# Kernel tuning notes

Hardware: AMD Instinct MI355X
Metric: run time of the kernel (lower is better)

The kernel has to match this reference:

```python
import jax, jax.numpy as jnp
import numpy as np

B, T, C, H = 16, 2048, 1024, 128  # BATCH_SIZE, BLOCK_SIZE, EMBEDDING_SIZE, HEAD_SIZE


def setup_inputs() -> dict:
    key = jax.random.key(0)
    kx, kk, kq, kv = jax.random.split(key, 4)
    x = jax.random.normal(kx, (B, T, C), dtype=jnp.float32)
    # torch Linear(C, H, bias=False): y = x @ W^T with W [H, C]; we store W^T as [C, H]
    scale = C ** -0.5
    Wk = jax.random.normal(kk, (C, H), dtype=jnp.float32) * scale
    Wq = jax.random.normal(kq, (C, H), dtype=jnp.float32) * scale
    Wv = jax.random.normal(kv, (C, H), dtype=jnp.float32) * scale
    return {"x": x, "Wk": Wk, "Wq": Wq, "Wv": Wv}


def reference(x, Wk, Wq, Wv):
    # projections: [B, T, H]
    k = jnp.einsum("btc,ch->bth", x, Wk)
    q = jnp.einsum("btc,ch->bth", x, Wq)
    v = jnp.einsum("btc,ch->bth", x, Wv)
    # scaled scores: [B, T, T]
    scores = jnp.einsum("bqh,bkh->bqk", q, k) * (H ** -0.5)
    # causal mask (tril) then softmax over keys
    causal = jnp.tril(jnp.ones((T, T), dtype=bool))
    scores = jnp.where(causal, scores, -jnp.inf)
    weights = jax.nn.softmax(scores, axis=-1)
    # dropout with p=0.0 is identity (eval mode)
    return jnp.einsum("bqk,bkh->bqh", weights, v)
```

## Files before the change

kernel.cpp:

```cpp
#include <hip/hip_runtime.h>
#include <cmath>

#define B_ 16
#define T_ 2048
#define C_ 1024
#define H_ 128

#define BQ 64
#define BK 64
#define PS 68

#define PM 64
#define PK 64

typedef __bf16 bf16;
typedef bf16 bf16x8 __attribute__((ext_vector_type(8)));
typedef bf16 bf16x4 __attribute__((ext_vector_type(4)));
typedef float f32x4 __attribute__((ext_vector_type(4)));

#define GL_LDS16(gptr, lptr)                                                     \
    __builtin_amdgcn_global_load_lds(                                            \
        (const __attribute__((address_space(1))) unsigned int*)(gptr),           \
        (__attribute__((address_space(3))) unsigned int*)(lptr), 16, 0, 0)

__global__ __launch_bounds__(256) void convert_w(
    const float* __restrict__ Wq, const float* __restrict__ Wk,
    const float* __restrict__ Wv, bf16* __restrict__ wt)
{
    int gid = blockIdx.x * 256 + threadIdx.x;
    int w   = gid >> 14;
    int rem = gid & 16383;
    int n   = rem >> 7;
    int k0  = (rem & 127) * 8;
    const float* src = (w == 0) ? Wq : (w == 1) ? Wk : Wv;
    bf16x8 o;
#pragma unroll
    for (int j = 0; j < 8; ++j) o[j] = (bf16)src[(size_t)(k0 + j) * H_ + n];
    *(bf16x8*)(wt + (size_t)w * (H_ * C_) + (size_t)n * C_ + k0) = o;
}

__global__ __launch_bounds__(256, 2) void proj_mfma(
    const float* __restrict__ x, const bf16* __restrict__ wt,
    bf16* __restrict__ qb, bf16* __restrict__ kb, bf16* __restrict__ vtp)
{
    __shared__ bf16 xs[PM * PK];
    __shared__ bf16 ws[3 * H_ * PK];

    const int tid  = threadIdx.x;
    const int wave = tid >> 6;
    const int lane = tid & 63;
    const int quad = lane >> 4;
    const int lq   = lane & 15;
    const int wr   = wave >> 1;
    const int wc   = wave & 1;
    const int m0   = blockIdx.x * PM;

    f32x4 acc[3][2][4];
#pragma unroll
    for (int w = 0; w < 3; ++w)
#pragma unroll
        for (int mt = 0; mt < 2; ++mt)
#pragma unroll
            for (int nt = 0; nt < 4; ++nt)
                acc[w][mt][nt] = (f32x4){0.f, 0.f, 0.f, 0.f};

    int woff[12];
#pragma unroll
    for (int j = 0; j < 12; ++j) {
        int s  = (wave * 12 + j) * 64 + lane;
        int w  = s >> 10;
        int n  = (s >> 3) & 127;
        int cs = s & 7;
        int c  = cs ^ (n & 7);
        woff[j] = w * (H_ * C_) + n * C_ + c * 8;
    }
    int xoff[4], xslot[4];
#pragma unroll
    for (int j = 0; j < 4; ++j) {
        int f4  = j * 256 + tid;
        int row = f4 >> 4;
        int c4  = f4 & 15;
        int c   = c4 >> 1, half = c4 & 1;
        xoff[j]  = (m0 + row) * C_ + c4 * 4;
        xslot[j] = (row * 8 + (c ^ (row & 7))) * 8 + half * 4;
    }

    for (int k0 = 0; k0 < C_; k0 += PK) {
        __syncthreads();
#pragma unroll
        for (int j = 0; j < 12; ++j) {
            GL_LDS16(wt + woff[j] + k0, (char*)ws + (wave * 12 + j) * 1024);
        }
#pragma unroll
        for (int j = 0; j < 4; ++j) {
            float4 v = *(const float4*)(x + (size_t)xoff[j] + k0);
            bf16x4 o = {(bf16)v.x, (bf16)v.y, (bf16)v.z, (bf16)v.w};
            *(bf16x4*)&xs[xslot[j]] = o;
        }
        __syncthreads();

#pragma unroll
        for (int kc = 0; kc < 2; ++kc) {
            const int c = kc * 4 + quad;
            bf16x8 af[2];
#pragma unroll
            for (int mt = 0; mt < 2; ++mt) {
                int row  = wr * 32 + mt * 16 + lq;
                int slot = row * 8 + (c ^ (row & 7));
                af[mt] = *(const bf16x8*)&xs[slot * 8];
            }
#pragma unroll
            for (int w = 0; w < 3; ++w) {
#pragma unroll
                for (int nt = 0; nt < 4; ++nt) {
                    int n    = wc * 64 + nt * 16 + lq;
                    int slot = n * 8 + (c ^ (n & 7));
                    bf16x8 bfr = *(const bf16x8*)&ws[w * (H_ * PK) + slot * 8];
                    acc[w][0][nt] = __builtin_amdgcn_mfma_f32_16x16x32_bf16(af[0], bfr, acc[w][0][nt], 0, 0, 0);
                    acc[w][1][nt] = __builtin_amdgcn_mfma_f32_16x16x32_bf16(af[1], bfr, acc[w][1][nt], 0, 0, 0);
                }
            }
        }
    }

    const int b  = m0 >> 11;
    const int t0 = m0 & (T_ - 1);
#pragma unroll
    for (int w = 0; w < 2; ++w) {
        bf16* dst = (w == 0) ? qb : kb;
#pragma unroll
        for (int mt = 0; mt < 2; ++mt)
#pragma unroll
            for (int nt = 0; nt < 4; ++nt)
#pragma unroll
                for (int r = 0; r < 4; ++r) {
                    int row = m0 + wr * 32 + mt * 16 + quad * 4 + r;
                    int h   = wc * 64 + nt * 16 + lq;
                    dst[(size_t)row * H_ + h] = (bf16)acc[w][mt][nt][r];
                }
    }
#pragma unroll
    for (int mt = 0; mt < 2; ++mt)
#pragma unroll
        for (int nt = 0; nt < 4; ++nt) {
            int h = wc * 64 + nt * 16 + lq;
            int t = t0 + wr * 32 + mt * 16 + quad * 4;
            bf16x4 o = {(bf16)acc[2][mt][nt][0], (bf16)acc[2][mt][nt][1],
                        (bf16)acc[2][mt][nt][2], (bf16)acc[2][mt][nt][3]};
            *(bf16x4*)&vtp[((size_t)b * H_ + h) * T_ + t] = o;
        }
}

__global__ __launch_bounds__(256) void attn_mfma(
    const bf16* __restrict__ qb, const bf16* __restrict__ kb,
    const bf16* __restrict__ vt, float* __restrict__ out)
{
    __shared__ bf16 Ks[2][BK * 128];
    __shared__ bf16 Vs[2][128 * BK];
    __shared__ bf16 Ps[4][16 * PS];

    const int tid  = threadIdx.x;
    const int wave = tid >> 6;
    const int lane = tid & 63;
    const int quad = lane >> 4;
    const int lq   = lane & 15;

    const int bid = blockIdx.x;
    const int b   = bid & 15;
    const int jq  = bid >> 4;
    const int t0b = (31 - jq) * BQ;
    const int qt0 = t0b + wave * 16;

    const bf16* qrow = qb + ((size_t)b * T_ + qt0 + lq) * H_ + quad * 8;
    bf16x8 qf[4];
#pragma unroll
    for (int c = 0; c < 4; ++c) qf[c] = *(const bf16x8*)(qrow + 32 * c);

    f32x4 acc[8];
#pragma unroll
    for (int i = 0; i < 8; ++i) acc[i] = (f32x4){0.f, 0.f, 0.f, 0.f};
    f32x4 l_acc = (f32x4){0.f, 0.f, 0.f, 0.f};

    bf16x8 ones;
#pragma unroll
    for (int j = 0; j < 8; ++j) ones[j] = (bf16)1.0f;

    const float SC2 = 0.12751749985029928f;
    const int ntiles = t0b / BK + 1;

    const bf16* Kg = kb + (size_t)b * T_ * H_;
    const bf16* Vg = vt + (size_t)b * H_ * T_;
    bf16* Pw = &Ps[wave][0];

    int koff[4], voff[4], dst8[4];
#pragma unroll
    for (int j = 0; j < 4; ++j) {
        int p   = (j * 4 + wave) * 64 + lane;
        int r   = p >> 4, pos = p & 15;
        int l   = (pos & 8) | ((pos & 7) ^ (r & 7));
        koff[j] = r * H_ + l * 8;
        int hh  = p >> 3, pos2 = p & 7;
        voff[j] = hh * T_ + (pos2 ^ (hh & 7)) * 8;
        dst8[j] = (j * 4 + wave) * 64 * 8;
    }
    int swk[4], swv[2];
#pragma unroll
    for (int c = 0; c < 4; ++c) {
        int l = quad + 4 * c;
        swk[c] = (l & 8) | ((l & 7) ^ (lq & 7));
    }
#pragma unroll
    for (int kc = 0; kc < 2; ++kc) swv[kc] = (quad + 4 * kc) ^ (lq & 7);

#pragma unroll
    for (int j = 0; j < 4; ++j) {
        GL_LDS16(Kg + (size_t)koff[j], &Ks[0][dst8[j]]);
        GL_LDS16(Vg + (size_t)voff[j], &Vs[0][dst8[j]]);
    }

    for (int kt = 0; kt < ntiles; ++kt) {
        __syncthreads();
        if (kt + 1 < ntiles) {
            const int k1 = (kt + 1) * BK;
            const int nb = (kt + 1) & 1;
#pragma unroll
            for (int j = 0; j < 4; ++j) {
                GL_LDS16(Kg + (size_t)k1 * H_ + koff[j], &Ks[nb][dst8[j]]);
                GL_LDS16(Vg + (size_t)(k1 + voff[j]),    &Vs[nb][dst8[j]]);
            }
        }
        const bf16* Kb = &Ks[kt & 1][0];
        const bf16* Vb = &Vs[kt & 1][0];
        const bool finalt = (kt == ntiles - 1);

#pragma unroll
        for (int ns = 0; ns < 4; ++ns) {
            if (!finalt || ns <= wave) {
                f32x4 sv = (f32x4){0.f, 0.f, 0.f, 0.f};
#pragma unroll
                for (int c = 0; c < 4; ++c) {
                    bf16x8 kf = *(const bf16x8*)&Kb[((ns * 16 + lq) * 16 + swk[c]) * 8];
                    sv = __builtin_amdgcn_mfma_f32_16x16x32_bf16(qf[c], kf, sv, 0, 0, 0);
                }
                if (finalt && ns == wave) {
#pragma unroll
                    for (int r = 0; r < 4; ++r) {
                        float p = (lq <= quad * 4 + r) ? exp2f(sv[r] * SC2) : 0.f;
                        Pw[(quad * 4 + r) * PS + ns * 16 + lq] = (bf16)p;
                    }
                } else {
#pragma unroll
                    for (int r = 0; r < 4; ++r) {
                        Pw[(quad * 4 + r) * PS + ns * 16 + lq] = (bf16)exp2f(sv[r] * SC2);
                    }
                }
            } else {
#pragma unroll
                for (int r = 0; r < 4; ++r)
                    Pw[(quad * 4 + r) * PS + ns * 16 + lq] = (bf16)0.f;
            }
        }

        bf16x8 pf[2];
#pragma unroll
        for (int kc = 0; kc < 2; ++kc)
            pf[kc] = *(const bf16x8*)&Pw[lq * PS + kc * 32 + quad * 8];

        l_acc = __builtin_amdgcn_mfma_f32_16x16x32_bf16(pf[0], ones, l_acc, 0, 0, 0);
        l_acc = __builtin_amdgcn_mfma_f32_16x16x32_bf16(pf[1], ones, l_acc, 0, 0, 0);

#pragma unroll
        for (int ht = 0; ht < 8; ++ht) {
#pragma unroll
            for (int kc = 0; kc < 2; ++kc) {
                bf16x8 vf = *(const bf16x8*)&Vb[((ht * 16 + lq) * 8 + swv[kc]) * 8];
                acc[ht] = __builtin_amdgcn_mfma_f32_16x16x32_bf16(pf[kc], vf, acc[ht], 0, 0, 0);
            }
        }
    }

    float inv[4];
#pragma unroll
    for (int r = 0; r < 4; ++r) inv[r] = 1.f / l_acc[r];
#pragma unroll
    for (int ht = 0; ht < 8; ++ht) {
#pragma unroll
        for (int r = 0; r < 4; ++r) {
            out[((size_t)b * T_ + qt0 + quad * 4 + r) * H_ + ht * 16 + lq] = acc[ht][r] * inv[r];
        }
    }
}

extern "C" void kernel_launch(void* const* d_in, const int* in_sizes, int n_in,
                              void* d_out, int out_size, void* d_ws, size_t ws_size,
                              hipStream_t stream) {
    const float* x  = (const float*)d_in[0];
    const float* Wk = (const float*)d_in[1];
    const float* Wq = (const float*)d_in[2];
    const float* Wv = (const float*)d_in[3];
    float* out = (float*)d_out;

    bf16* qb = (bf16*)d_ws;
    bf16* kb = qb + (size_t)B_ * T_ * H_;
    bf16* vt = kb + (size_t)B_ * T_ * H_;
    bf16* wt = vt + (size_t)B_ * T_ * H_;

    convert_w<<<192, 256, 0, stream>>>(Wq, Wk, Wv, wt);

    proj_mfma<<<(B_ * T_) / PM, 256, 0, stream>>>(x, wt, qb, kb, vt);

    attn_mfma<<<(T_ / BQ) * B_, 256, 0, stream>>>(qb, kb, vt, out);
}
```

Baseline: 278.7 us.

## Double-buffer projection kernel LDS tiles with register and async prefetch

Converts the QKV projection kernel's K-loop to a two-stage pipeline. Weight tiles for the next step are loaded into the alternate LDS buffer with global_load_lds, and x tiles are prefetched into registers and stored after the MFMA work. This drops one barrier per iteration and overlaps memory traffic with compute. Doubling the shared memory lowers the launch bound from two blocks per CU to one, which reduces occupancy.

```diff
diff --git a/kernel.cpp b/kernel.cpp
--- a/kernel.cpp
+++ b/kernel.cpp
@@ -39,12 +39,12 @@
     *(bf16x8*)(wt + (size_t)w * (H_ * C_) + (size_t)n * C_ + k0) = o;
 }
 
-__global__ __launch_bounds__(256, 2) void proj_mfma(
+__global__ __launch_bounds__(256, 1) void proj_mfma(
     const float* __restrict__ x, const bf16* __restrict__ wt,
     bf16* __restrict__ qb, bf16* __restrict__ kb, bf16* __restrict__ vtp)
 {
-    __shared__ bf16 xs[PM * PK];
-    __shared__ bf16 ws[3 * H_ * PK];
+    __shared__ bf16 xs[2][PM * PK];
+    __shared__ bf16 ws[2][3 * H_ * PK];
 
     const int tid  = threadIdx.x;
     const int wave = tid >> 6;
@@ -85,19 +85,33 @@
         xslot[j] = (row * 8 + (c ^ (row & 7))) * 8 + half * 4;
     }
 
-    for (int k0 = 0; k0 < C_; k0 += PK) {
+    float4 xv[4];
+#pragma unroll
+    for (int j = 0; j < 4; ++j) xv[j] = *(const float4*)(x + (size_t)xoff[j]);
+#pragma unroll
+    for (int j = 0; j < 12; ++j)
+        GL_LDS16(wt + woff[j], (char*)ws[0] + (wave * 12 + j) * 1024);
+#pragma unroll
+    for (int j = 0; j < 4; ++j) {
+        bf16x4 o = {(bf16)xv[j].x, (bf16)xv[j].y, (bf16)xv[j].z, (bf16)xv[j].w};
+        *(bf16x4*)&xs[0][xslot[j]] = o;
+    }
+
+    const int NT = C_ / PK;
+    for (int kt = 0; kt < NT; ++kt) {
         __syncthreads();
-#pragma unroll
-        for (int j = 0; j < 12; ++j) {
-            GL_LDS16(wt + woff[j] + k0, (char*)ws + (wave * 12 + j) * 1024);
-        }
-#pragma unroll
-        for (int j = 0; j < 4; ++j) {
-            float4 v = *(const float4*)(x + (size_t)xoff[j] + k0);
-            bf16x4 o = {(bf16)v.x, (bf16)v.y, (bf16)v.z, (bf16)v.w};
-            *(bf16x4*)&xs[xslot[j]] = o;
-        }
-        __syncthreads();
+        const int cur = kt & 1;
+        const bool pf = (kt + 1 < NT);
+
+        if (pf) {
+            const int k1 = (kt + 1) * PK;
+#pragma unroll
+            for (int j = 0; j < 4; ++j)
+                xv[j] = *(const float4*)(x + (size_t)xoff[j] + k1);
+#pragma unroll
+            for (int j = 0; j < 12; ++j)
+                GL_LDS16(wt + woff[j] + k1, (char*)ws[cur ^ 1] + (wave * 12 + j) * 1024);
+        }
 
 #pragma unroll
         for (int kc = 0; kc < 2; ++kc) {
@@ -107,7 +121,7 @@
             for (int mt = 0; mt < 2; ++mt) {
                 int row  = wr * 32 + mt * 16 + lq;
                 int slot = row * 8 + (c ^ (row & 7));
-                af[mt] = *(const bf16x8*)&xs[slot * 8];
+                af[mt] = *(const bf16x8*)&xs[cur][slot * 8];
             }
 #pragma unroll
             for (int w = 0; w < 3; ++w) {
@@ -115,10 +129,18 @@
                 for (int nt = 0; nt < 4; ++nt) {
                     int n    = wc * 64 + nt * 16 + lq;
                     int slot = n * 8 + (c ^ (n & 7));
-                    bf16x8 bfr = *(const bf16x8*)&ws[w * (H_ * PK) + slot * 8];
+                    bf16x8 bfr = *(const bf16x8*)&ws[cur][w * (H_ * PK) + slot * 8];
                     acc[w][0][nt] = __builtin_amdgcn_mfma_f32_16x16x32_bf16(af[0], bfr, acc[w][0][nt], 0, 0, 0);
                     acc[w][1][nt] = __builtin_amdgcn_mfma_f32_16x16x32_bf16(af[1], bfr, acc[w][1][nt], 0, 0, 0);
                 }
+            }
+        }
+
+        if (pf) {
+#pragma unroll
+            for (int j = 0; j < 4; ++j) {
+                bf16x4 o = {(bf16)xv[j].x, (bf16)xv[j].y, (bf16)xv[j].z, (bf16)xv[j].w};
+                *(bf16x4*)&xs[cur ^ 1][xslot[j]] = o;
             }
         }
     }
```

After: 311.5 us. +11.7%, slower.

## Double-buffer weight tiles and load x directly into MFMA fragments in projection

Applied to the files above, without the earlier changes.

Restructures the projection GEMM loop to use a 32-wide K step with double-buffered LDS for the weights. The next tile is prefetched through async global-to-LDS loads and register prefetch of x, so one barrier per step replaces two. x no longer goes through LDS: each lane loads its fp32 A-fragment directly, converts it to bf16 in registers, and feeds the MFMA. This aims to overlap memory with compute, but it halves the work per barrier, doubles the iteration count, and raises register pressure.

```diff
diff --git a/kernel.cpp b/kernel.cpp
--- a/kernel.cpp
+++ b/kernel.cpp
@@ -11,7 +11,7 @@
 #define PS 68
 
 #define PM 64
-#define PK 64
+#define PKW 32
 
 typedef __bf16 bf16;
 typedef bf16 bf16x8 __attribute__((ext_vector_type(8)));
@@ -43,8 +43,7 @@
     const float* __restrict__ x, const bf16* __restrict__ wt,
     bf16* __restrict__ qb, bf16* __restrict__ kb, bf16* __restrict__ vtp)
 {
-    __shared__ bf16 xs[PM * PK];
-    __shared__ bf16 ws[3 * H_ * PK];
+    __shared__ bf16 ws[2][3 * H_ * PKW];
 
     const int tid  = threadIdx.x;
     const int wave = tid >> 6;
@@ -64,63 +63,75 @@
             for (int nt = 0; nt < 4; ++nt)
                 acc[w][mt][nt] = (f32x4){0.f, 0.f, 0.f, 0.f};
 
-    int woff[12];
-#pragma unroll
-    for (int j = 0; j < 12; ++j) {
-        int s  = (wave * 12 + j) * 64 + lane;
-        int w  = s >> 10;
-        int n  = (s >> 3) & 127;
-        int cs = s & 7;
-        int c  = cs ^ (n & 7);
+    int woff[6];
+#pragma unroll
+    for (int j = 0; j < 6; ++j) {
+        int p  = (wave * 6 + j) * 64 + lane;
+        int ng = p >> 2;
+        int cs = p & 3;
+        int w  = ng >> 7;
+        int n  = ng & 127;
+        int sn = (n ^ (n >> 2)) & 3;
+        int c  = cs ^ sn;
         woff[j] = w * (H_ * C_) + n * C_ + c * 8;
     }
-    int xoff[4], xslot[4];
-#pragma unroll
-    for (int j = 0; j < 4; ++j) {
-        int f4  = j * 256 + tid;
-        int row = f4 >> 4;
-        int c4  = f4 & 15;
-        int c   = c4 >> 1, half = c4 & 1;
-        xoff[j]  = (m0 + row) * C_ + c4 * 4;
-        xslot[j] = (row * 8 + (c ^ (row & 7))) * 8 + half * 4;
-    }
-
-    for (int k0 = 0; k0 < C_; k0 += PK) {
+    int xoff[2];
+#pragma unroll
+    for (int mt = 0; mt < 2; ++mt)
+        xoff[mt] = (m0 + wr * 32 + mt * 16 + lq) * C_ + quad * 8;
+
+    float4 xr[2][2], xr2[2][2];
+#pragma unroll
+    for (int mt = 0; mt < 2; ++mt)
+#pragma unroll
+        for (int h = 0; h < 2; ++h)
+            xr[mt][h] = *(const float4*)(x + (size_t)xoff[mt] + h * 4);
+#pragma unroll
+    for (int j = 0; j < 6; ++j)
+        GL_LDS16(wt + woff[j], (char*)ws[0] + (wave * 6 + j) * 1024);
+
+    const int NT = C_ / PKW;
+    for (int kt = 0; kt < NT; ++kt) {
         __syncthreads();
-#pragma unroll
-        for (int j = 0; j < 12; ++j) {
-            GL_LDS16(wt + woff[j] + k0, (char*)ws + (wave * 12 + j) * 1024);
-        }
-#pragma unroll
-        for (int j = 0; j < 4; ++j) {
-            float4 v = *(const float4*)(x + (size_t)xoff[j] + k0);
-            bf16x4 o = {(bf16)v.x, (bf16)v.y, (bf16)v.z, (bf16)v.w};
-            *(bf16x4*)&xs[xslot[j]] = o;
-        }
-        __syncthreads();
-
-#pragma unroll
-        for (int kc = 0; kc < 2; ++kc) {
-            const int c = kc * 4 + quad;
-            bf16x8 af[2];
-#pragma unroll
-            for (int mt = 0; mt < 2; ++mt) {
-                int row  = wr * 32 + mt * 16 + lq;
-                int slot = row * 8 + (c ^ (row & 7));
-                af[mt] = *(const bf16x8*)&xs[slot * 8];
+        const int cur = kt & 1;
+        if (kt + 1 < NT) {
+            const int k1 = (kt + 1) * PKW;
+#pragma unroll
+            for (int mt = 0; mt < 2; ++mt)
+#pragma unroll
+                for (int h = 0; h < 2; ++h)
+                    xr2[mt][h] = *(const float4*)(x + (size_t)xoff[mt] + k1 + h * 4);
+#pragma unroll
+            for (int j = 0; j < 6; ++j)
+                GL_LDS16(wt + woff[j] + k1, (char*)ws[cur ^ 1] + (wave * 6 + j) * 1024);
+        }
+
+        bf16x8 af[2];
+#pragma unroll
+        for (int mt = 0; mt < 2; ++mt) {
+            af[mt][0] = (bf16)xr[mt][0].x; af[mt][1] = (bf16)xr[mt][0].y;
+            af[mt][2] = (bf16)xr[mt][0].z; af[mt][3] = (bf16)xr[mt][0].w;
+            af[mt][4] = (bf16)xr[mt][1].x; af[mt][5] = (bf16)xr[mt][1].y;
+            af[mt][6] = (bf16)xr[mt][1].z; af[mt][7] = (bf16)xr[mt][1].w;
+        }
+
+#pragma unroll
+        for (int w = 0; w < 3; ++w)
+#pragma unroll
+            for (int nt = 0; nt < 4; ++nt) {
+                int n    = wc * 64 + nt * 16 + lq;
+                int sn   = (n ^ (n >> 2)) & 3;
+                int slot = (w * 128 + n) * 4 + (quad ^ sn);
+                bf16x8 bfr = *(const bf16x8*)&ws[cur][slot * 8];
+                acc[w][0][nt] = __builtin_amdgcn_mfma_f32_16x16x32_bf16(af[0], bfr, acc[w][0][nt], 0, 0, 0);
+                acc[w][1][nt] = __builtin_amdgcn_mfma_f32_16x16x32_bf16(af[1], bfr, acc[w][1][nt], 0, 0, 0);
             }
-#pragma unroll
-            for (int w = 0; w < 3; ++w) {
-#pragma unroll
-                for (int nt = 0; nt < 4; ++nt) {
-                    int n    = wc * 64 + nt * 16 + lq;
-                    int slot = n * 8 + (c ^ (n & 7));
-                    bf16x8 bfr = *(const bf16x8*)&ws[w * (H_ * PK) + slot * 8];
-                    acc[w][0][nt] = __builtin_amdgcn_mfma_f32_16x16x32_bf16(af[0], bfr, acc[w][0][nt], 0, 0, 0);
-                    acc[w][1][nt] = __builtin_amdgcn_mfma_f32_16x16x32_bf16(af[1], bfr, acc[w][1][nt], 0, 0, 0);
-                }
-            }
-        }
+
+#pragma unroll
+        for (int mt = 0; mt < 2; ++mt)
+#pragma unroll
+            for (int h = 0; h < 2; ++h)
+                xr[mt][h] = xr2[mt][h];
     }
 
     const int b  = m0 >> 11;
```

Measured after the change: 292.7 us. +5.0%, slower.

## Split projection GEMM per weight matrix with larger 128-row M tiles

Applied to the files above, without the earlier changes.

The projection kernel now gives each block a single weight matrix (Q, K or V) and a 128-row tile of x, in place of all three weights for a 64-row tile. This cuts the LDS footprint and accumulator registers per block and gives each block more M-reuse of the weight tile. In exchange, each x tile is now read and converted from fp32 three times, once per weight block, which adds global traffic on x.

```diff
diff --git a/kernel.cpp b/kernel.cpp
--- a/kernel.cpp
+++ b/kernel.cpp
@@ -10,8 +10,8 @@
 #define BK 64
 #define PS 68
 
-#define PM 64
-#define PK 64
+#define QM 128
+#define QK 64
 
 typedef __bf16 bf16;
 typedef bf16 bf16x8 __attribute__((ext_vector_type(8)));
@@ -39,12 +39,12 @@
     *(bf16x8*)(wt + (size_t)w * (H_ * C_) + (size_t)n * C_ + k0) = o;
 }
 
-__global__ __launch_bounds__(256, 2) void proj_mfma(
+__global__ __launch_bounds__(256) void proj_mfma(
     const float* __restrict__ x, const bf16* __restrict__ wt,
     bf16* __restrict__ qb, bf16* __restrict__ kb, bf16* __restrict__ vtp)
 {
-    __shared__ bf16 xs[PM * PK];
-    __shared__ bf16 ws[3 * H_ * PK];
+    __shared__ bf16 As[QM * QK];
+    __shared__ bf16 Bs[H_ * QK];
 
     const int tid  = threadIdx.x;
     const int wave = tid >> 6;
@@ -53,102 +53,101 @@
     const int lq   = lane & 15;
     const int wr   = wave >> 1;
     const int wc   = wave & 1;
-    const int m0   = blockIdx.x * PM;
-
-    f32x4 acc[3][2][4];
-#pragma unroll
-    for (int w = 0; w < 3; ++w)
-#pragma unroll
-        for (int mt = 0; mt < 2; ++mt)
-#pragma unroll
-            for (int nt = 0; nt < 4; ++nt)
-                acc[w][mt][nt] = (f32x4){0.f, 0.f, 0.f, 0.f};
-
-    int woff[12];
-#pragma unroll
-    for (int j = 0; j < 12; ++j) {
-        int s  = (wave * 12 + j) * 64 + lane;
-        int w  = s >> 10;
-        int n  = (s >> 3) & 127;
-        int cs = s & 7;
-        int c  = cs ^ (n & 7);
-        woff[j] = w * (H_ * C_) + n * C_ + c * 8;
-    }
-    int xoff[4], xslot[4];
-#pragma unroll
-    for (int j = 0; j < 4; ++j) {
-        int f4  = j * 256 + tid;
-        int row = f4 >> 4;
-        int c4  = f4 & 15;
-        int c   = c4 >> 1, half = c4 & 1;
-        xoff[j]  = (m0 + row) * C_ + c4 * 4;
-        xslot[j] = (row * 8 + (c ^ (row & 7))) * 8 + half * 4;
-    }
-
-    for (int k0 = 0; k0 < C_; k0 += PK) {
+
+    const int bid = blockIdx.x;
+    const int w   = bid % 3;
+    const int mt  = bid / 3;
+    const int m0  = mt * QM;
+    const bf16* wg = wt + (size_t)w * (H_ * C_);
+
+    f32x4 acc[4][4];
+#pragma unroll
+    for (int i = 0; i < 4; ++i)
+#pragma unroll
+        for (int j = 0; j < 4; ++j) acc[i][j] = (f32x4){0.f, 0.f, 0.f, 0.f};
+
+    int bsrc[4];
+#pragma unroll
+    for (int r = 0; r < 4; ++r) {
+        int p  = r * 256 + tid;
+        int n  = p >> 3;
+        int c  = (p & 7) ^ (n & 7);
+        bsrc[r] = n * C_ + c * 8;
+    }
+    int asrc[4], aslot[4];
+#pragma unroll
+    for (int r = 0; r < 4; ++r) {
+        int s   = r * 256 + tid;
+        int row = s >> 3;
+        int c   = (s & 7) ^ (row & 7);
+        asrc[r]  = (m0 + row) * C_ + c * 8;
+        aslot[r] = s * 8;
+    }
+
+    for (int kt = 0; kt < C_ / QK; ++kt) {
+        const int k0 = kt * QK;
         __syncthreads();
 #pragma unroll
-        for (int j = 0; j < 12; ++j) {
-            GL_LDS16(wt + woff[j] + k0, (char*)ws + (wave * 12 + j) * 1024);
-        }
-#pragma unroll
-        for (int j = 0; j < 4; ++j) {
-            float4 v = *(const float4*)(x + (size_t)xoff[j] + k0);
-            bf16x4 o = {(bf16)v.x, (bf16)v.y, (bf16)v.z, (bf16)v.w};
-            *(bf16x4*)&xs[xslot[j]] = o;
+        for (int r = 0; r < 4; ++r)
+            GL_LDS16(wg + bsrc[r] + k0, (char*)Bs + r * 4096 + wave * 1024);
+#pragma unroll
+        for (int r = 0; r < 4; ++r) {
+            float4 v0 = *(const float4*)(x + (size_t)asrc[r] + k0);
+            float4 v1 = *(const float4*)(x + (size_t)asrc[r] + k0 + 4);
+            bf16x8 o = {(bf16)v0.x, (bf16)v0.y, (bf16)v0.z, (bf16)v0.w,
+                        (bf16)v1.x, (bf16)v1.y, (bf16)v1.z, (bf16)v1.w};
+            *(bf16x8*)&As[aslot[r]] = o;
         }
         __syncthreads();
 
 #pragma unroll
         for (int kc = 0; kc < 2; ++kc) {
             const int c = kc * 4 + quad;
-            bf16x8 af[2];
-#pragma unroll
-            for (int mt = 0; mt < 2; ++mt) {
-                int row  = wr * 32 + mt * 16 + lq;
-                int slot = row * 8 + (c ^ (row & 7));
-                af[mt] = *(const bf16x8*)&xs[slot * 8];
-            }
-#pragma unroll
-            for (int w = 0; w < 3; ++w) {
-#pragma unroll
-                for (int nt = 0; nt < 4; ++nt) {
-                    int n    = wc * 64 + nt * 16 + lq;
-                    int slot = n * 8 + (c ^ (n & 7));
-                    bf16x8 bfr = *(const bf16x8*)&ws[w * (H_ * PK) + slot * 8];
-                    acc[w][0][nt] = __builtin_amdgcn_mfma_f32_16x16x32_bf16(af[0], bfr, acc[w][0][nt], 0, 0, 0);
-                    acc[w][1][nt] = __builtin_amdgcn_mfma_f32_16x16x32_bf16(af[1], bfr, acc[w][1][nt], 0, 0, 0);
-                }
-            }
+            bf16x8 af[4], bfr[4];
+#pragma unroll
+            for (int i = 0; i < 4; ++i) {
+                int row = wr * 64 + i * 16 + lq;
+                af[i] = *(const bf16x8*)&As[(row * 8 + (c ^ (row & 7))) * 8];
+            }
+#pragma unroll
+            for (int j = 0; j < 4; ++j) {
+                int n = wc * 64 + j * 16 + lq;
+                bfr[j] = *(const bf16x8*)&Bs[(n * 8 + (c ^ (n & 7))) * 8];
+            }
+#pragma unroll
+            for (int i = 0; i < 4; ++i)
+#pragma unroll
+                for (int j = 0; j < 4; ++j)
+                    acc[i][j] = __builtin_amdgcn_mfma_f32_16x16x32_bf16(af[i], bfr[j], acc[i][j], 0, 0, 0);
         }
     }
 
     const int b  = m0 >> 11;
     const int t0 = m0 & (T_ - 1);
-#pragma unroll
-    for (int w = 0; w < 2; ++w) {
+    if (w < 2) {
         bf16* dst = (w == 0) ? qb : kb;
 #pragma unroll
-        for (int mt = 0; mt < 2; ++mt)
-#pragma unroll
-            for (int nt = 0; nt < 4; ++nt)
+        for (int i = 0; i < 4; ++i)
+#pragma unroll
+            for (int j = 0; j < 4; ++j)
 #pragma unroll
                 for (int r = 0; r < 4; ++r) {
-                    int row = m0 + wr * 32 + mt * 16 + quad * 4 + r;
-                    int h   = wc * 64 + nt * 16 + lq;
-                    dst[(size_t)row * H_ + h] = (bf16)acc[w][mt][nt][r];
+                    int row = m0 + wr * 64 + i * 16 + quad * 4 + r;
+                    int h   = wc * 64 + j * 16 + lq;
+                    dst[(size_t)row * H_ + h] = (bf16)acc[i][j][r];
                 }
-    }
-#pragma unroll
-    for (int mt = 0; mt < 2; ++mt)
-#pragma unroll
-        for (int nt = 0; nt < 4; ++nt) {
-            int h = wc * 64 + nt * 16 + lq;
-            int t = t0 + wr * 32 + mt * 16 + quad * 4;
-            bf16x4 o = {(bf16)acc[2][mt][nt][0], (bf16)acc[2][mt][nt][1],
-                        (bf16)acc[2][mt][nt][2], (bf16)acc[2][mt][nt][3]};
-            *(bf16x4*)&vtp[((size_t)b * H_ + h) * T_ + t] = o;
-        }
+    } else {
+#pragma unroll
+        for (int i = 0; i < 4; ++i)
+#pragma unroll
+            for (int j = 0; j < 4; ++j) {
+                int h = wc * 64 + j * 16 + lq;
+                int t = t0 + wr * 64 + i * 16 + quad * 4;
+                bf16x4 o = {(bf16)acc[i][j][0], (bf16)acc[i][j][1],
+                            (bf16)acc[i][j][2], (bf16)acc[i][j][3]};
+                *(bf16x4*)&vtp[((size_t)b * H_ + h) * T_ + t] = o;
+            }
+    }
 }
 
 __global__ __launch_bounds__(256) void attn_mfma(
@@ -307,7 +306,7 @@
 
     convert_w<<<192, 256, 0, stream>>>(Wq, Wk, Wv, wt);
 
-    proj_mfma<<<(B_ * T_) / PM, 256, 0, stream>>>(x, wt, qb, kb, vt);
+    proj_mfma<<<(B_ * T_ / QM) * 3, 256, 0, stream>>>(x, wt, qb, kb, vt);
 
     attn_mfma<<<(T_ / BQ) * B_, 256, 0, stream>>>(qb, kb, vt, out);
 }
```

Result: slower. 290.8 us (+4.3%).
